# Kernel tuning notes

Hardware: AMD Instinct MI355X
Metric: run time of the kernel (lower is better)

## Reference

```python
import jax, jax.numpy as jnp
import numpy as np

L = 8      # num_hidden_layers
J = 3      # num_gnn_layers
N = 2000   # num nodes (<=2000 so prune=False)
E = 32000  # num edges
R = 64     # num relations
HID = 1024 # hidden_dim
G = 128    # gnn_dim
H = 8      # num_gnn_heads
DH = G // H          # 16 per-head dim
P = 10               # pre_seq_len
KV = 8               # plm_num_kv_heads
OUT = HID // 32 * KV # out_ft_dim = 256
B = 16               # batch (h.shape[0])


def setup_inputs() -> dict:
    key = jax.random.key(0)
    ks = jax.random.split(key, 24)
    f = lambda k, s: (jax.random.normal(k, s, dtype=jnp.float32) * 0.05)
    ri = lambda k, s, hi: jax.random.randint(k, s, 0, hi, dtype=jnp.int32)
    return {
        'nft': f(ks[0], (L, N, HID)),
        'rft': f(ks[1], (L, R, HID)),
        'importances': jax.random.normal(ks[2], (N,), dtype=jnp.float32),
        'tg_w': f(ks[3], (L, HID, G)),
        'tg_b': f(ks[4], (L, G)),
        'path_w': f(ks[5], (L, J, 3 * G, G)),
        'path_b': f(ks[6], (L, J, G)),
        'attn1_w': f(ks[7], (L, J, G, H)),
        'attn2_p': f(ks[8], (L, J, H, DH)),
        'trans_w': f(ks[9], (L, G, 2 * OUT)),
        'trans_b': f(ks[10], (L, 2 * OUT)),
        'lamda': jnp.zeros((L - 1,), dtype=jnp.float32),
        'edge_src': ri(ks[11], (E,), N),
        'edge_dst': ri(ks[12], (E,), N),
        'edge_label': ri(ks[13], (E,), R),
        'h': ri(ks[14], (B,), N),
        't': ri(ks[15], (B,), N),
    }


def _gat(x, eft, src, dst, Wp, bp, Wa1, a2p):
    # x: [N, G], eft: [E, G]
    ns = x[src]                       # [E, G] gather src node feats
    ne = x[dst]                       # [E, G] gather dst node feats
    epaths = (jnp.concatenate([ns, eft, ne], axis=-1) @ Wp + bp)
    epaths = epaths.reshape(E, H, DH)           # per-edge multi-head features
    a1 = ns @ Wa1                               # [E, H]
    a2 = jnp.einsum('ehd,hd->eh', epaths, a2p)  # [E, H]
    a = jax.nn.leaky_relu(a1 + a2)              # slope 0.01, matches torch default
    # edge softmax grouped by destination node
    amax = jax.ops.segment_max(a, dst, num_segments=N)
    ex = jnp.exp(a - amax[dst])
    ssum = jax.ops.segment_sum(ex, dst, num_segments=N)
    attn = ex / ssum[dst]                       # [E, H]
    msg = epaths * attn[..., None]              # [E, H, DH]
    agg = jax.ops.segment_sum(msg, dst, num_segments=N)  # [N, H, DH]
    return jax.nn.relu(agg.reshape(N, G) + x)


def reference(nft, rft, importances, tg_w, tg_b, path_w, path_b, attn1_w,
              attn2_p, trans_w, trans_b, lamda, edge_src, edge_dst,
              edge_label, h, t):
    bsz = h.shape[0]
    # topk indices of node importances (prune=False path)
    _, imp_idx = jax.lax.top_k(importances, P)
    pkv = []
    for i in range(L):
        x = nft[i] @ tg_w[i] + tg_b[i]                       # [N, G]
        # linear-then-gather == gather-then-linear (same math, less traffic)
        rel = rft[i] @ tg_w[i] + tg_b[i]                     # [R, G]
        gnn_eft = rel[edge_label]                            # [E, G]
        for j in range(J):
            x = _gat(x, gnn_eft, edge_src, edge_dst,
                     path_w[i, j], path_b[i, j], attn1_w[i, j], attn2_p[i, j])
        past_x = x
        if i > 0:
            s = jax.nn.sigmoid(lamda[i - 1] / 0.1)
            x = s * x + (1.0 - s) * past_x   # past_x == x (as in source)
        prefix = x[imp_idx]                                  # [P, G]
        pk = jnp.tanh(prefix) @ trans_w[i] + trans_b[i]      # [P, 2*OUT]
        pk = jnp.broadcast_to(pk[None], (bsz, P, 2 * OUT))
        pk = pk.reshape(bsz, P, 2, KV, OUT // KV).transpose(2, 0, 3, 1, 4)
        pkv.append(pk)
    return jnp.stack(pkv)   # [L, 2, B, KV, P, OUT//KV]
```

## Files before the change

### kernel.cpp

```cpp
#include <hip/hip_runtime.h>
#include <hip/hip_bf16.h>
#include <math.h>

#define L_    8
#define J_    3
#define N_    2000
#define E_    32000
#define R_    64
#define HID_  1024
#define G_    128
#define H_    8
#define DH_   16
#define P_    10
#define KV_   8
#define OUT2_ 512
#define B_    16
#define KS_   4
#define ROWS_ 2064

typedef float f32x4 __attribute__((ext_vector_type(4)));
typedef short s16x8 __attribute__((ext_vector_type(8)));

__device__ __forceinline__ void cvt_split1(float v, short& h, short& l) {
    unsigned u = __float_as_uint(v);
    h = (short)(u >> 16);
    float rem = v - __uint_as_float(u & 0xffff0000u);
    l = (short)(__float_as_uint(rem) >> 16);
}

__device__ __forceinline__ void cvt_split8(const float* v, s16x8& h, s16x8& l) {
    #pragma unroll
    for (int i = 0; i < 8; ++i) {
        unsigned u = __float_as_uint(v[i]);
        h[i] = (short)(u >> 16);
        float rem = v[i] - __uint_as_float(u & 0xffff0000u);
        l[i] = (short)(__float_as_uint(rem) >> 16);
    }
}

__global__ void k_deg(const int* __restrict__ dst, int* __restrict__ deg) {
    int e = blockIdx.x * 256 + threadIdx.x;
    if (e < E_) atomicAdd(&deg[dst[e]], 1);
}

__global__ __launch_bounds__(256) void k_scan(const int* __restrict__ deg, int* __restrict__ off) {
    __shared__ int ps[256];
    int t = threadIdx.x;
    int base = t * 8;
    int v[8];
    int sum = 0;
    #pragma unroll
    for (int j = 0; j < 8; ++j) {
        int idx = base + j;
        int d = (idx < N_) ? deg[idx] : 0;
        v[j] = sum;
        sum += d;
    }
    ps[t] = sum;
    __syncthreads();
    for (int st = 1; st < 256; st <<= 1) {
        int x = (t >= st) ? ps[t - st] : 0;
        __syncthreads();
        ps[t] += x;
        __syncthreads();
    }
    int pre = (t == 0) ? 0 : ps[t - 1];
    #pragma unroll
    for (int j = 0; j < 8; ++j) {
        int idx = base + j;
        if (idx <= N_) off[idx] = pre + v[j];
    }
}

__global__ void k_place(const int* __restrict__ dst, const int* __restrict__ src,
                        const int* __restrict__ lab, const int* __restrict__ off,
                        int* __restrict__ cur, int2* __restrict__ sl) {
    int e = blockIdx.x * 256 + threadIdx.x;
    if (e < E_) {
        int n = dst[e];
        int slot = atomicAdd(&cur[n], 1);
        sl[off[n] + slot] = make_int2(src[e], lab[e]);
    }
}

__global__ void k_topk(const float* __restrict__ imp, int* __restrict__ idx_out) {
    __shared__ float sv[N_];
    __shared__ float rv[256];
    __shared__ int   ri[256];
    int t = threadIdx.x;
    for (int i = t; i < N_; i += 256) sv[i] = imp[i];
    __syncthreads();
    for (int k = 0; k < P_; ++k) {
        float bv = -INFINITY; int bi = N_;
        for (int i = t; i < N_; i += 256) {
            float v = sv[i];
            if (v > bv || (v == bv && i < bi)) { bv = v; bi = i; }
        }
        rv[t] = bv; ri[t] = bi;
        __syncthreads();
        for (int s = 128; s > 0; s >>= 1) {
            if (t < s) {
                float v = rv[t + s]; int i2 = ri[t + s];
                if (v > rv[t] || (v == rv[t] && i2 < ri[t])) { rv[t] = v; ri[t] = i2; }
            }
            __syncthreads();
        }
        if (t == 0) { idx_out[k] = ri[0]; sv[ri[0]] = -INFINITY; }
        __syncthreads();
    }
}

__global__ __launch_bounds__(256) void k_wsplit(
    const float* __restrict__ tg_w, short* __restrict__ Wpk) {
    int layer = blockIdx.x >> 5;
    int st = blockIdx.x & 31;
    int tid = threadIdx.x;
    int col = tid & 127, khalf = tid >> 7;
    const float* src = tg_w + (size_t)layer * HID_ * G_ + (size_t)(st * 32 + khalf * 16) * G_ + col;
    short* dh = Wpk + ((size_t)(layer * 32 + st) * 2 + 0) * 4096 + tid * 16;
    short* dl = Wpk + ((size_t)(layer * 32 + st) * 2 + 1) * 4096 + tid * 16;
    #pragma unroll
    for (int kk = 0; kk < 16; ++kk) {
        short h, l;
        cvt_split1(src[(size_t)kk * G_], h, l);
        dh[kk] = h; dl[kk] = l;
    }
}

__global__ __launch_bounds__(256) void k_psplit(
    const float* __restrict__ path_w, short* __restrict__ Ppk) {
    int lj = blockIdx.x >> 3;
    int rest = blockIdx.x & 7;
    int halfc = rest >> 2;
    int st = rest & 3;
    int tid = threadIdx.x;
    int col = tid & 127, khalf = tid >> 7;
    int c0 = halfc ? 256 : 0;
    const float* src = path_w + (size_t)lj * 384 * G_ + (size_t)(c0 + st * 32 + khalf * 16) * G_ + col;
    size_t base = (((size_t)lj * 2 + halfc) * 4 + st) * 2;
    short* dh = Ppk + (base + 0) * 4096 + tid * 16;
    short* dl = Ppk + (base + 1) * 4096 + tid * 16;
    #pragma unroll
    for (int kk = 0; kk < 16; ++kk) {
        short h, l;
        cvt_split1(src[(size_t)kk * G_], h, l);
        dh[kk] = h; dl[kk] = l;
    }
}

#define TG_NS 8
__global__ __launch_bounds__(256) void k_tgA(
    const float* __restrict__ nft, const float* __restrict__ rft,
    const short* __restrict__ Wpk, float* __restrict__ part) {
    __shared__ alignas(16) short Ah[64][40];
    __shared__ alignas(16) short Al[64][40];
    __shared__ alignas(16) short Wh[128][40];
    __shared__ alignas(16) short Wl[128][40];
    const int tid = threadIdx.x;
    const int rg = blockIdx.x % 33;
    const int t2 = blockIdx.x / 33;
    const int layer = t2 % L_;
    const int ks = t2 / L_;
    const int row0 = rg * 64;
    const int k0 = ks * (HID_ / KS_);

    const int arow = tid >> 2, aq = tid & 3;
    int gra = row0 + arow; if (gra > ROWS_ - 1) gra = ROWS_ - 1;
    const float* asrc = (gra < N_)
        ? nft + ((size_t)layer * N_ + gra) * HID_ + k0
        : rft + ((size_t)layer * R_ + (gra - N_)) * HID_ + k0;
    const int wcol = tid & 127, wkh = tid >> 7;

    const int lane = tid & 63, wv = tid >> 6;
    const int lr = lane & 15, lk = (lane >> 4) * 8;

    f32x4 zero = {0.f, 0.f, 0.f, 0.f};
    f32x4 acc[4][2];
    #pragma unroll
    for (int i = 0; i < 4; ++i) { acc[i][0] = zero; acc[i][1] = zero; }

    float aa[8];
    s16x8 wh0, wh1, wl0, wl1;
    auto ldG = [&](int st) {
        int kk0 = st * 32;
        *(float4*)&aa[0] = *(const float4*)(asrc + kk0 + aq * 8);
        *(float4*)&aa[4] = *(const float4*)(asrc + kk0 + aq * 8 + 4);
        int gst = ks * TG_NS + st;
        const s16x8* ph = (const s16x8*)(Wpk + ((size_t)(layer * 32 + gst) * 2 + 0) * 4096 + tid * 16);
        const s16x8* pl = (const s16x8*)(Wpk + ((size_t)(layer * 32 + gst) * 2 + 1) * 4096 + tid * 16);
        wh0 = ph[0]; wh1 = ph[1];
        wl0 = pl[0]; wl1 = pl[1];
    };
    ldG(0);
    for (int st = 0; st < TG_NS; ++st) {
        __syncthreads();
        {
            s16x8 h, l; cvt_split8(aa, h, l);
            *(s16x8*)&Ah[arow][aq * 8] = h;
            *(s16x8*)&Al[arow][aq * 8] = l;
            *(s16x8*)&Wh[wcol][wkh * 16]     = wh0;
            *(s16x8*)&Wh[wcol][wkh * 16 + 8] = wh1;
            *(s16x8*)&Wl[wcol][wkh * 16]     = wl0;
            *(s16x8*)&Wl[wcol][wkh * 16 + 8] = wl1;
        }
        __syncthreads();
        if (st + 1 < TG_NS) ldG(st + 1);
        s16x8 bh[2], bl[2];
        #pragma unroll
        for (int c = 0; c < 2; ++c) {
            int col = wv * 32 + c * 16 + lr;
            bh[c] = *(s16x8*)&Wh[col][lk];
            bl[c] = *(s16x8*)&Wl[col][lk];
        }
        #pragma unroll
        for (int mf = 0; mf < 4; ++mf) {
            s16x8 ah = *(s16x8*)&Ah[mf * 16 + lr][lk];
            s16x8 al = *(s16x8*)&Al[mf * 16 + lr][lk];
            #pragma unroll
            for (int c = 0; c < 2; ++c) {
                acc[mf][c] = __builtin_amdgcn_mfma_f32_16x16x32_bf16(ah, bh[c], acc[mf][c], 0, 0, 0);
                acc[mf][c] = __builtin_amdgcn_mfma_f32_16x16x32_bf16(ah, bl[c], acc[mf][c], 0, 0, 0);
                acc[mf][c] = __builtin_amdgcn_mfma_f32_16x16x32_bf16(al, bh[c], acc[mf][c], 0, 0, 0);
            }
        }
    }
    float* dst = part + (size_t)(ks * L_ + layer) * ROWS_ * G_;
    const int rbase = (lane >> 4) * 4;
    #pragma unroll
    for (int mf = 0; mf < 4; ++mf) {
        #pragma unroll
        for (int c = 0; c < 2; ++c) {
            int col = wv * 32 + c * 16 + lr;
            #pragma unroll
            for (int rgi = 0; rgi < 4; ++rgi) {
                int row = row0 + mf * 16 + rbase + rgi;
                if (row < ROWS_) dst[(size_t)row * G_ + col] = acc[mf][c][rgi];
            }
        }
    }
}

__global__ __launch_bounds__(256) void k_tred(
    const float* __restrict__ part, const float* __restrict__ tg_b,
    float* __restrict__ x0, float* __restrict__ rel) {
    int f4 = blockIdx.x * 256 + threadIdx.x;
    int layer = f4 / (ROWS_ * 32);
    int rem = f4 % (ROWS_ * 32);
    int row = rem >> 5;
    int c4 = rem & 31;
    const float4* p = (const float4*)part;
    size_t stride = (size_t)L_ * ROWS_ * 32;
    size_t idx0 = ((size_t)layer * ROWS_ + row) * 32 + c4;
    float4 s0 = p[idx0];
    float4 s1 = p[idx0 + stride];
    float4 s2 = p[idx0 + 2 * stride];
    float4 s3 = p[idx0 + 3 * stride];
    float4 b = *(const float4*)(tg_b + layer * G_ + c4 * 4);
    float4 o;
    o.x = s0.x + s1.x + s2.x + s3.x + b.x;
    o.y = s0.y + s1.y + s2.y + s3.y + b.y;
    o.z = s0.z + s1.z + s2.z + s3.z + b.z;
    o.w = s0.w + s1.w + s2.w + s3.w + b.w;
    if (row < N_) ((float4*)x0)[((size_t)layer * N_ + row) * 32 + c4] = o;
    else          ((float4*)rel)[((size_t)layer * R_ + (row - N_)) * 32 + c4] = o;
}

__global__ __launch_bounds__(256) void k_prep(
    const float* __restrict__ path_w, const float* __restrict__ path_b,
    const float* __restrict__ attn1_w, const float* __restrict__ attn2_p,
    float* __restrict__ wPR, short* __restrict__ PPk, float* __restrict__ bA) {
    int j = blockIdx.x / L_;
    int l = blockIdx.x % L_;
    int t = threadIdx.x;
    size_t wb = (size_t)((l * J_ + j) * 384) * G_;
    size_t ob = (size_t)(j * L_ + l);
    const float* a2 = attn2_p + (size_t)(l * J_ + j) * G_;
    short* pph = PPk + (ob * 2 + 0) * 2048;
    short* ppl = PPk + (ob * 2 + 1) * 2048;
    for (int i = t; i < G_ * H_; i += 256) {
        int k = i >> 3, h = i & 7;
        const float* a2h = a2 + h * DH_;
        float s1 = 0.f, s2 = 0.f, s3 = 0.f;
        for (int d = 0; d < DH_; ++d) {
            float av = a2h[d];
            int c = h * DH_ + d;
            s1 += path_w[wb + (size_t)k * G_ + c] * av;
            s3 += path_w[wb + (size_t)(128 + k) * G_ + c] * av;
            s2 += path_w[wb + (size_t)(256 + k) * G_ + c] * av;
        }
        s1 += attn1_w[((size_t)(l * J_ + j) * G_ + k) * H_ + h];
        short h1, l1, h2, l2;
        cvt_split1(s1, h1, l1);
        cvt_split1(s2, h2, l2);
        pph[h * 128 + k] = h1;       ppl[h * 128 + k] = l1;
        pph[(8 + h) * 128 + k] = h2; ppl[(8 + h) * 128 + k] = l2;
        wPR[ob * H_ * G_ + h * G_ + k] = s3;
    }
    if (t < H_) {
        float s = 0.f;
        const float* a2h = a2 + t * DH_;
        const float* pb = path_b + (size_t)(l * J_ + j) * G_ + t * DH_;
        for (int d = 0; d < DH_; ++d) s += pb[d] * a2h[d];
        bA[ob * H_ + t] = s;
    }
}

__global__ __launch_bounds__(256) void k_rel(
    const float* __restrict__ rel, const float* __restrict__ path_w,
    const float* __restrict__ wPR, float* __restrict__ Rl, float* __restrict__ PR) {
    __shared__ float At[32][132];
    __shared__ float Wt[32][132];
    const int tid = threadIdx.x;
    const int halfb = blockIdx.x & 1;
    const int t2 = blockIdx.x >> 1;
    const int l = t2 % L_;
    const int j = t2 / L_;
    const int row0 = halfb * 32;
    const size_t ob = (size_t)(j * L_ + l);
    {
        int ar = tid >> 3, aq2 = tid & 7;
        const float* asrc = rel + ((size_t)l * R_ + row0 + ar) * G_ + aq2 * 16;
        float4 a0 = ((const float4*)asrc)[0], a1 = ((const float4*)asrc)[1];
        float4 a2 = ((const float4*)asrc)[2], a3 = ((const float4*)asrc)[3];
        *(float4*)&At[ar][aq2 * 16]      = a0;
        *(float4*)&At[ar][aq2 * 16 + 4]  = a1;
        *(float4*)&At[ar][aq2 * 16 + 8]  = a2;
        *(float4*)&At[ar][aq2 * 16 + 12] = a3;
    }
    const size_t wb = (size_t)((l * J_ + j) * 384) * G_;
    const int wrow = tid >> 3, wq = tid & 7;
    float4 rW0, rW1, rW2, rW3;
    auto loadW = [&](int kt) {
        const float* src = path_w + wb + (size_t)(128 + kt * 32 + wrow) * G_ + wq * 16;
        rW0 = ((const float4*)src)[0]; rW1 = ((const float4*)src)[1];
        rW2 = ((const float4*)src)[2]; rW3 = ((const float4*)src)[3];
    };
    const int tr = tid >> 4;
    const int tc = tid & 15;
    float4 acc[2][2];
    acc[0][0] = make_float4(0, 0, 0, 0); acc[0][1] = make_float4(0, 0, 0, 0);
    acc[1][0] = make_float4(0, 0, 0, 0); acc[1][1] = make_float4(0, 0, 0, 0);
    loadW(0);
    for (int wt = 0; wt < 4; ++wt) {
        __syncthreads();
        *(float4*)&Wt[wrow][wq * 16]      = rW0;
        *(float4*)&Wt[wrow][wq * 16 + 4]  = rW1;
        *(float4*)&Wt[wrow][wq * 16 + 8]  = rW2;
        *(float4*)&Wt[wrow][wq * 16 + 12] = rW3;
        __syncthreads();
        if (wt + 1 < 4) loadW(wt + 1);
        #pragma unroll
        for (int kk = 0; kk < 32; ++kk) {
            float4 w0 = *(const float4*)&Wt[kk][tc * 4];
            float4 w1 = *(const float4*)&Wt[kk][64 + tc * 4];
            float a0 = At[tr * 2][wt * 32 + kk];
            float a1 = At[tr * 2 + 1][wt * 32 + kk];
            acc[0][0].x += a0 * w0.x; acc[0][0].y += a0 * w0.y;
            acc[0][0].z += a0 * w0.z; acc[0][0].w += a0 * w0.w;
            acc[0][1].x += a0 * w1.x; acc[0][1].y += a0 * w1.y;
            acc[0][1].z += a0 * w1.z; acc[0][1].w += a0 * w1.w;
            acc[1][0].x += a1 * w0.x; acc[1][0].y += a1 * w0.y;
            acc[1][0].z += a1 * w0.z; acc[1][0].w += a1 * w0.w;
            acc[1][1].x += a1 * w1.x; acc[1][1].y += a1 * w1.y;
            acc[1][1].z += a1 * w1.z; acc[1][1].w += a1 * w1.w;
        }
    }
    #pragma unroll
    for (int r2 = 0; r2 < 2; ++r2) {
        int row = row0 + tr * 2 + r2;
        float* dst = Rl + (ob * R_ + row) * G_;
        *(float4*)(dst + tc * 4) = acc[r2][0];
        *(float4*)(dst + 64 + tc * 4) = acc[r2][1];
    }
    {
        int prow = tid >> 3, ph = tid & 7;
        const float* wp = wPR + (ob * H_ + ph) * G_;
        float s = 0.f;
        for (int k = 0; k < G_; ++k) s += At[prow][k] * wp[k];
        PR[(ob * R_ + row0 + prow) * H_ + ph] = s;
    }
}

__global__ __launch_bounds__(256) void k_proj2(
    const float* __restrict__ xcur, const short* __restrict__ Ppk,
    const short* __restrict__ PPkj, const float* __restrict__ bAj,
    const float* __restrict__ path_b, int j,
    float* __restrict__ Xs, float* __restrict__ XdB,
    float* __restrict__ PS, float* __restrict__ PDb) {
    __shared__ alignas(16) short Ah[64][40];
    __shared__ alignas(16) short Al[64][40];
    __shared__ alignas(16) short Wh[128][40];
    __shared__ alignas(16) short Wl[128][40];
    __shared__ alignas(16) short PPh[16][136];
    __shared__ alignas(16) short PPl[16][136];
    const int tid = threadIdx.x;
    const int layer = blockIdx.x & 7;
    const int rest = blockIdx.x >> 3;
    const int halfb = rest & 1;
    const int rg = rest >> 1;
    const int row0 = rg * 64;

    const int arow = tid >> 2, aq = tid & 3;
    int gra = row0 + arow; if (gra >= N_) gra = N_ - 1;
    const float* asrc = xcur + ((size_t)layer * N_ + gra) * G_;
    const int wcol = tid & 127, wkh = tid >> 7;

    const int lane = tid & 63, wv = tid >> 6;
    const int lr = lane & 15, lk = (lane >> 4) * 8;

    if (!halfb) {
        int col = tid >> 4, koff = (tid & 15) * 8;
        s16x8 vh = *(const s16x8*)(PPkj + ((size_t)layer * 2 + 0) * 2048 + tid * 8);
        s16x8 vl = *(const s16x8*)(PPkj + ((size_t)layer * 2 + 1) * 2048 + tid * 8);
        *(s16x8*)&PPh[col][koff] = vh;
        *(s16x8*)&PPl[col][koff] = vl;
    }

    f32x4 zero = {0.f, 0.f, 0.f, 0.f};
    f32x4 acc[4][2];
    f32x4 acc_pp[2];
    #pragma unroll
    for (int i = 0; i < 4; ++i) { acc[i][0] = zero; acc[i][1] = zero; }
    acc_pp[0] = zero; acc_pp[1] = zero;

    float aa[8];
    s16x8 wh0, wh1, wl0, wl1;
    const size_t pbase = (((size_t)(layer * J_ + j) * 2 + halfb) * 4) * 2;
    auto ldG = [&](int st) {
        int kk0 = st * 32;
        *(float4*)&aa[0] = *(const float4*)(asrc + kk0 + aq * 8);
        *(float4*)&aa[4] = *(const float4*)(asrc + kk0 + aq * 8 + 4);
        const s16x8* ph = (const s16x8*)(Ppk + (pbase + (size_t)st * 2 + 0) * 4096 + tid * 16);
        const s16x8* pl = (const s16x8*)(Ppk + (pbase + (size_t)st * 2 + 1) * 4096 + tid * 16);
        wh0 = ph[0]; wh1 = ph[1];
        wl0 = pl[0]; wl1 = pl[1];
    };
    ldG(0);
    for (int st = 0; st < 4; ++st) {
        __syncthreads();
        {
            s16x8 h, l; cvt_split8(aa, h, l);
            *(s16x8*)&Ah[arow][aq * 8] = h;
            *(s16x8*)&Al[arow][aq * 8] = l;
            *(s16x8*)&Wh[wcol][wkh * 16]     = wh0;
            *(s16x8*)&Wh[wcol][wkh * 16 + 8] = wh1;
            *(s16x8*)&Wl[wcol][wkh * 16]     = wl0;
            *(s16x8*)&Wl[wcol][wkh * 16 + 8] = wl1;
        }
        __syncthreads();
        if (st + 1 < 4) ldG(st + 1);
        s16x8 bh[2], bl[2];
        #pragma unroll
        for (int c = 0; c < 2; ++c) {
            int col = wv * 32 + c * 16 + lr;
            bh[c] = *(s16x8*)&Wh[col][lk];
            bl[c] = *(s16x8*)&Wl[col][lk];
        }
        s16x8 ppb_h, ppb_l;
        if (!halfb) {
            ppb_h = *(s16x8*)&PPh[lr][st * 32 + lk];
            ppb_l = *(s16x8*)&PPl[lr][st * 32 + lk];
        }
        #pragma unroll
        for (int mf = 0; mf < 4; ++mf) {
            s16x8 ah = *(s16x8*)&Ah[mf * 16 + lr][lk];
            s16x8 al = *(s16x8*)&Al[mf * 16 + lr][lk];
            #pragma unroll
            for (int c = 0; c < 2; ++c) {
                acc[mf][c] = __builtin_amdgcn_mfma_f32_16x16x32_bf16(ah, bh[c], acc[mf][c], 0, 0, 0);
                acc[mf][c] = __builtin_amdgcn_mfma_f32_16x16x32_bf16(ah, bl[c], acc[mf][c], 0, 0, 0);
                acc[mf][c] = __builtin_amdgcn_mfma_f32_16x16x32_bf16(al, bh[c], acc[mf][c], 0, 0, 0);
            }
            if (!halfb && (mf >> 1) == wv) {
                int i = mf & 1;
                acc_pp[i] = __builtin_amdgcn_mfma_f32_16x16x32_bf16(ah, ppb_h, acc_pp[i], 0, 0, 0);
                acc_pp[i] = __builtin_amdgcn_mfma_f32_16x16x32_bf16(ah, ppb_l, acc_pp[i], 0, 0, 0);
                acc_pp[i] = __builtin_amdgcn_mfma_f32_16x16x32_bf16(al, ppb_h, acc_pp[i], 0, 0, 0);
            }
        }
    }
    const float* pb = path_b + (size_t)(layer * J_ + j) * G_;
    float* outp = halfb ? XdB : Xs;
    const int rbase = (lane >> 4) * 4;
    #pragma unroll
    for (int mf = 0; mf < 4; ++mf) {
        #pragma unroll
        for (int c = 0; c < 2; ++c) {
            int col = wv * 32 + c * 16 + lr;
            float bias = halfb ? pb[col] : 0.f;
            #pragma unroll
            for (int rgi = 0; rgi < 4; ++rgi) {
                int row = row0 + mf * 16 + rbase + rgi;
                if (row < N_) outp[((size_t)layer * N_ + row) * G_ + col] = acc[mf][c][rgi] + bias;
            }
        }
    }
    if (!halfb) {
        #pragma unroll
        for (int i = 0; i < 2; ++i) {
            int mf = wv * 2 + i;
            #pragma unroll
            for (int rgi = 0; rgi < 4; ++rgi) {
                int row = row0 + mf * 16 + rbase + rgi;
                if (row >= N_) continue;
                float val = acc_pp[i][rgi];
                if (lr < 8) PS[((size_t)layer * N_ + row) * H_ + lr] = val;
                else        PDb[((size_t)layer * N_ + row) * H_ + (lr - 8)] = val + bAj[layer * H_ + (lr - 8)];
            }
        }
    }
}

__global__ __launch_bounds__(256) void k_node(
    const float* __restrict__ xcur, const float* __restrict__ Xs,
    const float* __restrict__ XdB, const float* __restrict__ Rlj,
    const float* __restrict__ PS, const float* __restrict__ PDb,
    const float* __restrict__ PRj,
    const int* __restrict__ off, const int2* __restrict__ csr_sl,
    float* __restrict__ xnext) {
    int l = blockIdx.x & 7;
    int n = (blockIdx.x >> 3) * 4 + (threadIdx.x >> 6);
    int lane = threadIdx.x & 63;
    int o0 = off[n], o1 = off[n + 1];
    const float* xr = xcur + ((size_t)l * N_ + n) * G_;
    float xv0 = xr[lane], xv1 = xr[lane + 64];
    float xd0 = XdB[((size_t)l * N_ + n) * G_ + lane];
    float xd1 = XdB[((size_t)l * N_ + n) * G_ + lane + 64];
    float out0, out1;
    if (o1 == o0) {
        out0 = fmaxf(xv0, 0.f);
        out1 = fmaxf(xv1, 0.f);
    } else {
        const int h0 = lane >> 4, h1 = h0 + 4;
        const float pd0 = PDb[((size_t)l * N_ + n) * H_ + h0];
        const float pd1 = PDb[((size_t)l * N_ + n) * H_ + h1];
        const float* PSl = PS + (size_t)l * N_ * H_;
        const float* PRl = PRj + (size_t)l * R_ * H_;
        const float* Xsl = Xs + (size_t)l * N_ * G_;
        const float* Rll = Rlj + (size_t)l * R_ * G_;
        float acc0 = 0.f, acc1 = 0.f, sum0 = 0.f, sum1 = 0.f;
        #pragma unroll 2
        for (int k = o0; k < o1; ++k) {
            int2 sl = csr_sl[k];
            float lg0 = PSl[sl.x * H_ + h0] + PRl[sl.y * H_ + h0] + pd0;
            float lg1 = PSl[sl.x * H_ + h1] + PRl[sl.y * H_ + h1] + pd1;
            lg0 = (lg0 >= 0.f) ? lg0 : 0.01f * lg0;
            lg1 = (lg1 >= 0.f) ? lg1 : 0.01f * lg1;
            float e0 = __expf(lg0), e1 = __expf(lg1);
            float v0 = Xsl[(size_t)sl.x * G_ + lane]      + Rll[(size_t)sl.y * G_ + lane];
            float v1 = Xsl[(size_t)sl.x * G_ + lane + 64] + Rll[(size_t)sl.y * G_ + lane + 64];
            acc0 += e0 * v0; sum0 += e0;
            acc1 += e1 * v1; sum1 += e1;
        }
        out0 = fmaxf(acc0 / sum0 + xd0 + xv0, 0.f);
        out1 = fmaxf(acc1 / sum1 + xd1 + xv1, 0.f);
    }
    float* dst = xnext + ((size_t)l * N_ + n) * G_;
    dst[lane] = out0;
    dst[lane + 64] = out1;
}

__global__ __launch_bounds__(256) void k_out(
    const float* __restrict__ xfin, const int* __restrict__ imp_idx,
    const float* __restrict__ trans_w, const float* __restrict__ trans_b,
    float* __restrict__ out) {
    int blk = blockIdx.x;
    int layer = blk / P_, p = blk % P_;
    __shared__ float th[G_];
    int t = threadIdx.x;
    int row = imp_idx[p];
    if (t < G_) th[t] = tanhf(xfin[((size_t)layer * N_ + row) * G_ + t]);
    __syncthreads();
    for (int c = t; c < OUT2_; c += 256) {
        float s = trans_b[layer * OUT2_ + c];
        const float* W = trans_w + (size_t)layer * G_ * OUT2_ + c;
        for (int k = 0; k < G_; ++k) s += th[k] * W[(size_t)k * OUT2_];
        int c2 = c >> 8, kv = (c >> 5) & 7, oo = c & 31;
        for (int b = 0; b < B_; ++b) {
            out[(((((size_t)layer * 2 + c2) * B_ + b) * KV_ + kv) * P_ + p) * 32 + oo] = s;
        }
    }
}

extern "C" void kernel_launch(void* const* d_in, const int* in_sizes, int n_in,
                              void* d_out, int out_size, void* d_ws, size_t ws_size,
                              hipStream_t stream) {
    const float* nft     = (const float*)d_in[0];
    const float* rft     = (const float*)d_in[1];
    const float* imp     = (const float*)d_in[2];
    const float* tg_w    = (const float*)d_in[3];
    const float* tg_b    = (const float*)d_in[4];
    const float* path_w  = (const float*)d_in[5];
    const float* path_b  = (const float*)d_in[6];
    const float* attn1_w = (const float*)d_in[7];
    const float* attn2_p = (const float*)d_in[8];
    const float* trans_w = (const float*)d_in[9];
    const float* trans_b = (const float*)d_in[10];
    const int* esrc = (const int*)d_in[12];
    const int* edst = (const int*)d_in[13];
    const int* elab = (const int*)d_in[14];
    float* out = (float*)d_out;

    char* w = (char*)d_ws;
    size_t off = 0;
    auto alloc = [&](size_t bytes) {
        void* p = w + off;
        off += (bytes + 255) & ~(size_t)255;
        return p;
    };
    float* part    = (float*)alloc((size_t)KS_ * L_ * ROWS_ * G_ * 4);
    float* x0      = (float*)alloc((size_t)L_ * N_ * G_ * 4);
    float* x1      = (float*)alloc((size_t)L_ * N_ * G_ * 4);
    float* rel     = (float*)alloc((size_t)L_ * R_ * G_ * 4);
    float* Xs      = (float*)alloc((size_t)L_ * N_ * G_ * 4);
    float* XdB     = (float*)alloc((size_t)L_ * N_ * G_ * 4);
    float* Rl      = (float*)alloc((size_t)J_ * L_ * R_ * G_ * 4);
    float* PS      = (float*)alloc((size_t)L_ * N_ * H_ * 4);
    float* PDb     = (float*)alloc((size_t)L_ * N_ * H_ * 4);
    float* PR      = (float*)alloc((size_t)J_ * L_ * R_ * H_ * 4);
    float* wPR     = (float*)alloc((size_t)J_ * L_ * H_ * G_ * 4);
    float* bA      = (float*)alloc((size_t)J_ * L_ * H_ * 4);
    short* Wpk     = (short*)alloc((size_t)L_ * 32 * 2 * 4096 * 2);
    short* Ppk     = (short*)alloc((size_t)L_ * J_ * 2 * 4 * 2 * 4096 * 2);
    short* PPk     = (short*)alloc((size_t)J_ * L_ * 2 * 2048 * 2);
    int*   deg     = (int*)alloc(N_ * 4);
    int*   cur     = (int*)alloc(N_ * 4);
    int*   csr_off = (int*)alloc((N_ + 1) * 4);
    int2*  csr_sl  = (int2*)alloc((size_t)E_ * 8);
    int*   imp_idx = (int*)alloc(P_ * 4);

    hipMemsetAsync(deg, 0, N_ * 4, stream);
    hipMemsetAsync(cur, 0, N_ * 4, stream);

    k_deg<<<E_ / 256, 256, 0, stream>>>(edst, deg);
    k_scan<<<1, 256, 0, stream>>>(deg, csr_off);
    k_place<<<E_ / 256, 256, 0, stream>>>(edst, esrc, elab, csr_off, cur, csr_sl);
    k_topk<<<1, 256, 0, stream>>>(imp, imp_idx);

    k_wsplit<<<L_ * 32, 256, 0, stream>>>(tg_w, Wpk);
    k_psplit<<<L_ * J_ * 2 * 4, 256, 0, stream>>>(path_w, Ppk);

    k_tgA<<<KS_ * L_ * 33, 256, 0, stream>>>(nft, rft, Wpk, part);
    k_tred<<<2064, 256, 0, stream>>>(part, tg_b, x0, rel);

    k_prep<<<J_ * L_, 256, 0, stream>>>(path_w, path_b, attn1_w, attn2_p,
                                        wPR, PPk, bA);
    k_rel<<<J_ * L_ * 2, 256, 0, stream>>>(rel, path_w, wPR, Rl, PR);

    float* xc = x0;
    float* xn = x1;
    for (int j = 0; j < J_; ++j) {
        k_proj2<<<L_ * 32 * 2, 256, 0, stream>>>(
            xc, Ppk, PPk + (size_t)j * L_ * 2 * 2048, bA + (size_t)j * L_ * H_,
            path_b, j, Xs, XdB, PS, PDb);
        k_node<<<L_ * 500, 256, 0, stream>>>(
            xc, Xs, XdB, Rl + (size_t)j * L_ * R_ * G_, PS, PDb,
            PR + (size_t)j * L_ * R_ * H_,
            csr_off, csr_sl, xn);
        float* tmp = xc; xc = xn; xn = tmp;
    }
    k_out<<<L_ * P_, 256, 0, stream>>>(xc, imp_idx, trans_w, trans_b, out);
}
```

Baseline: 227.6 us.

## Merge preprocessing kernels and replace split-K tg GEMM with direct-register full-K MFMA

```diff
diff --git a/kernel.cpp b/kernel.cpp
--- a/kernel.cpp
+++ b/kernel.cpp
@@ -15,7 +15,6 @@
 #define KV_   8
 #define OUT2_ 512
 #define B_    16
-#define KS_   4
 #define ROWS_ 2064
 
 typedef float f32x4 __attribute__((ext_vector_type(4)));
@@ -38,12 +37,27 @@
     }
 }
 
-__global__ void k_deg(const int* __restrict__ dst, int* __restrict__ deg) {
-    int e = blockIdx.x * 256 + threadIdx.x;
+__device__ __forceinline__ void cvt_split8v(float4 a, float4 b, s16x8& h, s16x8& l) {
+    short hh, ll;
+    cvt_split1(a.x, hh, ll); h[0] = hh; l[0] = ll;
+    cvt_split1(a.y, hh, ll); h[1] = hh; l[1] = ll;
+    cvt_split1(a.z, hh, ll); h[2] = hh; l[2] = ll;
+    cvt_split1(a.w, hh, ll); h[3] = hh; l[3] = ll;
+    cvt_split1(b.x, hh, ll); h[4] = hh; l[4] = ll;
+    cvt_split1(b.y, hh, ll); h[5] = hh; l[5] = ll;
+    cvt_split1(b.z, hh, ll); h[6] = hh; l[6] = ll;
+    cvt_split1(b.w, hh, ll); h[7] = hh; l[7] = ll;
+}
+
+
+__device__ __forceinline__ void deg_body(int b, const int* __restrict__ dst,
+                                         int* __restrict__ deg) {
+    int e = b * 256 + threadIdx.x;
     if (e < E_) atomicAdd(&deg[dst[e]], 1);
 }
 
-__global__ __launch_bounds__(256) void k_scan(const int* __restrict__ deg, int* __restrict__ off) {
+__device__ __forceinline__ void scan_body(const int* __restrict__ deg,
+                                          int* __restrict__ off) {
     __shared__ int ps[256];
     int t = threadIdx.x;
     int base = t * 8;
@@ -72,10 +86,13 @@
     }
 }
 
-__global__ void k_place(const int* __restrict__ dst, const int* __restrict__ src,
-                        const int* __restrict__ lab, const int* __restrict__ off,
-                        int* __restrict__ cur, int2* __restrict__ sl) {
-    int e = blockIdx.x * 256 + threadIdx.x;
+__device__ __forceinline__ void place_body(int b, const int* __restrict__ dst,
+                                           const int* __restrict__ src,
+                                           const int* __restrict__ lab,
+                                           const int* __restrict__ off,
+                                           int* __restrict__ cur,
+                                           int2* __restrict__ sl) {
+    int e = b * 256 + threadIdx.x;
     if (e < E_) {
         int n = dst[e];
         int slot = atomicAdd(&cur[n], 1);
@@ -83,7 +100,8 @@
     }
 }
 
-__global__ void k_topk(const float* __restrict__ imp, int* __restrict__ idx_out) {
+__device__ __forceinline__ void topk_body(const float* __restrict__ imp,
+                                          int* __restrict__ idx_out) {
     __shared__ float sv[N_];
     __shared__ float rv[256];
     __shared__ int   ri[256];
@@ -110,15 +128,15 @@
     }
 }
 
-__global__ __launch_bounds__(256) void k_wsplit(
-    const float* __restrict__ tg_w, short* __restrict__ Wpk) {
-    int layer = blockIdx.x >> 5;
-    int st = blockIdx.x & 31;
+__device__ __forceinline__ void wsplitB_body(int b, const float* __restrict__ tg_w,
+                                             short* __restrict__ WpkB) {
+    int layer = b >> 5;
+    int gst = b & 31;
     int tid = threadIdx.x;
     int col = tid & 127, khalf = tid >> 7;
-    const float* src = tg_w + (size_t)layer * HID_ * G_ + (size_t)(st * 32 + khalf * 16) * G_ + col;
-    short* dh = Wpk + ((size_t)(layer * 32 + st) * 2 + 0) * 4096 + tid * 16;
-    short* dl = Wpk + ((size_t)(layer * 32 + st) * 2 + 1) * 4096 + tid * 16;
+    const float* src = tg_w + ((size_t)layer * HID_ + gst * 32 + khalf * 16) * G_ + col;
+    short* dh = WpkB + ((size_t)(layer * 32 + gst) * 2 + 0) * 4096 + col * 32 + khalf * 16;
+    short* dl = WpkB + ((size_t)(layer * 32 + gst) * 2 + 1) * 4096 + col * 32 + khalf * 16;
     #pragma unroll
     for (int kk = 0; kk < 16; ++kk) {
         short h, l;
@@ -127,10 +145,10 @@
     }
 }
 
-__global__ __launch_bounds__(256) void k_psplit(
-    const float* __restrict__ path_w, short* __restrict__ Ppk) {
-    int lj = blockIdx.x >> 3;
-    int rest = blockIdx.x & 7;
+__device__ __forceinline__ void psplit_body(int b, const float* __restrict__ path_w,
+                                            short* __restrict__ Ppk) {
+    int lj = b >> 3;
+    int rest = b & 7;
     int halfc = rest >> 2;
     int st = rest & 3;
     int tid = threadIdx.x;
@@ -148,129 +166,15 @@
     }
 }
 
-#define TG_NS 8
-__global__ __launch_bounds__(256) void k_tgA(
-    const float* __restrict__ nft, const float* __restrict__ rft,
-    const short* __restrict__ Wpk, float* __restrict__ part) {
-    __shared__ alignas(16) short Ah[64][40];
-    __shared__ alignas(16) short Al[64][40];
-    __shared__ alignas(16) short Wh[128][40];
-    __shared__ alignas(16) short Wl[128][40];
-    const int tid = threadIdx.x;
-    const int rg = blockIdx.x % 33;
-    const int t2 = blockIdx.x / 33;
-    const int layer = t2 % L_;
-    const int ks = t2 / L_;
-    const int row0 = rg * 64;
-    const int k0 = ks * (HID_ / KS_);
-
-    const int arow = tid >> 2, aq = tid & 3;
-    int gra = row0 + arow; if (gra > ROWS_ - 1) gra = ROWS_ - 1;
-    const float* asrc = (gra < N_)
-        ? nft + ((size_t)layer * N_ + gra) * HID_ + k0
-        : rft + ((size_t)layer * R_ + (gra - N_)) * HID_ + k0;
-    const int wcol = tid & 127, wkh = tid >> 7;
-
-    const int lane = tid & 63, wv = tid >> 6;
-    const int lr = lane & 15, lk = (lane >> 4) * 8;
-
-    f32x4 zero = {0.f, 0.f, 0.f, 0.f};
-    f32x4 acc[4][2];
-    #pragma unroll
-    for (int i = 0; i < 4; ++i) { acc[i][0] = zero; acc[i][1] = zero; }
-
-    float aa[8];
-    s16x8 wh0, wh1, wl0, wl1;
-    auto ldG = [&](int st) {
-        int kk0 = st * 32;
-        *(float4*)&aa[0] = *(const float4*)(asrc + kk0 + aq * 8);
-        *(float4*)&aa[4] = *(const float4*)(asrc + kk0 + aq * 8 + 4);
-        int gst = ks * TG_NS + st;
-        const s16x8* ph = (const s16x8*)(Wpk + ((size_t)(layer * 32 + gst) * 2 + 0) * 4096 + tid * 16);
-        const s16x8* pl = (const s16x8*)(Wpk + ((size_t)(layer * 32 + gst) * 2 + 1) * 4096 + tid * 16);
-        wh0 = ph[0]; wh1 = ph[1];
-        wl0 = pl[0]; wl1 = pl[1];
-    };
-    ldG(0);
-    for (int st = 0; st < TG_NS; ++st) {
-        __syncthreads();
-        {
-            s16x8 h, l; cvt_split8(aa, h, l);
-            *(s16x8*)&Ah[arow][aq * 8] = h;
-            *(s16x8*)&Al[arow][aq * 8] = l;
-            *(s16x8*)&Wh[wcol][wkh * 16]     = wh0;
-            *(s16x8*)&Wh[wcol][wkh * 16 + 8] = wh1;
-            *(s16x8*)&Wl[wcol][wkh * 16]     = wl0;
-            *(s16x8*)&Wl[wcol][wkh * 16 + 8] = wl1;
-        }
-        __syncthreads();
-        if (st + 1 < TG_NS) ldG(st + 1);
-        s16x8 bh[2], bl[2];
-        #pragma unroll
-        for (int c = 0; c < 2; ++c) {
-            int col = wv * 32 + c * 16 + lr;
-            bh[c] = *(s16x8*)&Wh[col][lk];
-            bl[c] = *(s16x8*)&Wl[col][lk];
-        }
-        #pragma unroll
-        for (int mf = 0; mf < 4; ++mf) {
-            s16x8 ah = *(s16x8*)&Ah[mf * 16 + lr][lk];
-            s16x8 al = *(s16x8*)&Al[mf * 16 + lr][lk];
-            #pragma unroll
-            for (int c = 0; c < 2; ++c) {
-                acc[mf][c] = __builtin_amdgcn_mfma_f32_16x16x32_bf16(ah, bh[c], acc[mf][c], 0, 0, 0);
-                acc[mf][c] = __builtin_amdgcn_mfma_f32_16x16x32_bf16(ah, bl[c], acc[mf][c], 0, 0, 0);
-                acc[mf][c] = __builtin_amdgcn_mfma_f32_16x16x32_bf16(al, bh[c], acc[mf][c], 0, 0, 0);
-            }
-        }
-    }
-    float* dst = part + (size_t)(ks * L_ + layer) * ROWS_ * G_;
-    const int rbase = (lane >> 4) * 4;
-    #pragma unroll
-    for (int mf = 0; mf < 4; ++mf) {
-        #pragma unroll
-        for (int c = 0; c < 2; ++c) {
-            int col = wv * 32 + c * 16 + lr;
-            #pragma unroll
-            for (int rgi = 0; rgi < 4; ++rgi) {
-                int row = row0 + mf * 16 + rbase + rgi;
-                if (row < ROWS_) dst[(size_t)row * G_ + col] = acc[mf][c][rgi];
-            }
-        }
-    }
-}
-
-__global__ __launch_bounds__(256) void k_tred(
-    const float* __restrict__ part, const float* __restrict__ tg_b,
-    float* __restrict__ x0, float* __restrict__ rel) {
-    int f4 = blockIdx.x * 256 + threadIdx.x;
-    int layer = f4 / (ROWS_ * 32);
-    int rem = f4 % (ROWS_ * 32);
-    int row = rem >> 5;
-    int c4 = rem & 31;
-    const float4* p = (const float4*)part;
-    size_t stride = (size_t)L_ * ROWS_ * 32;
-    size_t idx0 = ((size_t)layer * ROWS_ + row) * 32 + c4;
-    float4 s0 = p[idx0];
-    float4 s1 = p[idx0 + stride];
-    float4 s2 = p[idx0 + 2 * stride];
-    float4 s3 = p[idx0 + 3 * stride];
-    float4 b = *(const float4*)(tg_b + layer * G_ + c4 * 4);
-    float4 o;
-    o.x = s0.x + s1.x + s2.x + s3.x + b.x;
-    o.y = s0.y + s1.y + s2.y + s3.y + b.y;
-    o.z = s0.z + s1.z + s2.z + s3.z + b.z;
-    o.w = s0.w + s1.w + s2.w + s3.w + b.w;
-    if (row < N_) ((float4*)x0)[((size_t)layer * N_ + row) * 32 + c4] = o;
-    else          ((float4*)rel)[((size_t)layer * R_ + (row - N_)) * 32 + c4] = o;
-}
-
-__global__ __launch_bounds__(256) void k_prep(
-    const float* __restrict__ path_w, const float* __restrict__ path_b,
-    const float* __restrict__ attn1_w, const float* __restrict__ attn2_p,
-    float* __restrict__ wPR, short* __restrict__ PPk, float* __restrict__ bA) {
-    int j = blockIdx.x / L_;
-    int l = blockIdx.x % L_;
+__device__ __forceinline__ void prep_body(int b, const float* __restrict__ path_w,
+                                          const float* __restrict__ path_b,
+                                          const float* __restrict__ attn1_w,
+                                          const float* __restrict__ attn2_p,
+                                          float* __restrict__ wPR,
+                                          short* __restrict__ PPk,
+                                          float* __restrict__ bA) {
+    int j = b / L_;
+    int l = b % L_;
     int t = threadIdx.x;
     size_t wb = (size_t)((l * J_ + j) * 384) * G_;
     size_t ob = (size_t)(j * L_ + l);
@@ -303,6 +207,132 @@
         for (int d = 0; d < DH_; ++d) s += pb[d] * a2h[d];
         bA[ob * H_ + t] = s;
     }
+}
+
+__device__ __forceinline__ void tg_body(
+    int b, const float* __restrict__ nft, const float* __restrict__ rft,
+    const short* __restrict__ WpkB, const float* __restrict__ tg_b,
+    float* __restrict__ x0, float* __restrict__ rel) {
+    const int layer = b & 7;
+    const int rg = b >> 3;
+    const int row0 = rg * 32;
+    const int tid = threadIdx.x;
+    const int lane = tid & 63, wv = tid >> 6;
+    const int lr = lane & 15, kg = lane >> 4;
+
+    const float* aptr[2];
+    #pragma unroll
+    for (int mf = 0; mf < 2; ++mf) {
+        int r = row0 + mf * 16 + lr;
+        if (r > ROWS_ - 1) r = ROWS_ - 1;
+        aptr[mf] = (r < N_)
+            ? nft + ((size_t)layer * N_ + r) * HID_ + kg * 8
+            : rft + ((size_t)layer * R_ + (r - N_)) * HID_ + kg * 8;
+    }
+    const short* bptr = WpkB + (size_t)layer * 32 * 8192 + (wv * 32 + lr) * 32 + kg * 8;
+
+    f32x4 zero = {0.f, 0.f, 0.f, 0.f};
+    f32x4 acc[2][2];
+    acc[0][0] = zero; acc[0][1] = zero; acc[1][0] = zero; acc[1][1] = zero;
+
+    float4 a4[2][2][2];
+    s16x8  bb[2][2][2];
+
+#define TG_LOAD(S, GST) do { \
+    _Pragma("unroll") \
+    for (int mf_ = 0; mf_ < 2; ++mf_) { \
+        const float4* p4_ = (const float4*)(aptr[mf_] + (size_t)(GST) * 32); \
+        a4[S][mf_][0] = p4_[0]; \
+        a4[S][mf_][1] = p4_[1]; \
+    } \
+    const short* bp_ = bptr + (size_t)(GST) * 8192; \
+    _Pragma("unroll") \
+    for (int n_ = 0; n_ < 2; ++n_) { \
+        _Pragma("unroll") \
+        for (int p_ = 0; p_ < 2; ++p_) \
+            bb[S][n_][p_] = *(const s16x8*)(bp_ + p_ * 4096 + n_ * 512); \
+    } \
+} while (0)
+
+#define TG_COMP(S) do { \
+    _Pragma("unroll") \
+    for (int mf_ = 0; mf_ < 2; ++mf_) { \
+        s16x8 ah_, al_; \
+        cvt_split8v(a4[S][mf_][0], a4[S][mf_][1], ah_, al_); \
+        _Pragma("unroll") \
+        for (int n_ = 0; n_ < 2; ++n_) { \
+            acc[mf_][n_] = __builtin_amdgcn_mfma_f32_16x16x32_bf16(ah_, bb[S][n_][0], acc[mf_][n_], 0, 0, 0); \
+            acc[mf_][n_] = __builtin_amdgcn_mfma_f32_16x16x32_bf16(ah_, bb[S][n_][1], acc[mf_][n_], 0, 0, 0); \
+            acc[mf_][n_] = __builtin_amdgcn_mfma_f32_16x16x32_bf16(al_, bb[S][n_][0], acc[mf_][n_], 0, 0, 0); \
+        } \
+    } \
+} while (0)
+
+    TG_LOAD(0, 0);
+    for (int t = 0; t < 30; t += 2) {
+        TG_LOAD(1, t + 1);
+        TG_COMP(0);
+        TG_LOAD(0, t + 2);
+        TG_COMP(1);
+    }
+    TG_LOAD(1, 31);
+    TG_COMP(0);
+    TG_COMP(1);
+#undef TG_LOAD
+#undef TG_COMP
+
+    const int rb = kg * 4;
+    #pragma unroll
+    for (int n = 0; n < 2; ++n) {
+        int col = wv * 32 + n * 16 + lr;
+        float bias = tg_b[layer * G_ + col];
+        #pragma unroll
+        for (int mf = 0; mf < 2; ++mf) {
+            #pragma unroll
+            for (int rgi = 0; rgi < 4; ++rgi) {
+                int row = row0 + mf * 16 + rb + rgi;
+                if (row >= ROWS_) continue;
+                float v = acc[mf][n][rgi] + bias;
+                if (row < N_) x0[((size_t)layer * N_ + row) * G_ + col] = v;
+                else          rel[((size_t)layer * R_ + (row - N_)) * G_ + col] = v;
+            }
+        }
+    }
+}
+
+
+__global__ __launch_bounds__(256) void k_pre1(
+    const int* __restrict__ edst, const float* __restrict__ imp,
+    const float* __restrict__ tg_w, const float* __restrict__ path_w,
+    int* __restrict__ deg, int* __restrict__ imp_idx,
+    short* __restrict__ WpkB, short* __restrict__ Ppk) {
+    int b = blockIdx.x;
+    if (b < 125) { deg_body(b, edst, deg); return; }
+    if (b == 125) { topk_body(imp, imp_idx); return; }
+    if (b < 382) { wsplitB_body(b - 126, tg_w, WpkB); return; }
+    psplit_body(b - 382, path_w, Ppk);
+}
+
+__global__ __launch_bounds__(256) void k_pre2(
+    const int* __restrict__ deg, const float* __restrict__ path_w,
+    const float* __restrict__ path_b, const float* __restrict__ attn1_w,
+    const float* __restrict__ attn2_p, int* __restrict__ csr_off,
+    float* __restrict__ wPR, short* __restrict__ PPk, float* __restrict__ bA) {
+    int b = blockIdx.x;
+    if (b == 0) { scan_body(deg, csr_off); return; }
+    prep_body(b - 1, path_w, path_b, attn1_w, attn2_p, wPR, PPk, bA);
+}
+
+__global__ __launch_bounds__(256) void k_pre3(
+    const int* __restrict__ edst, const int* __restrict__ esrc,
+    const int* __restrict__ elab, const int* __restrict__ off,
+    int* __restrict__ cur, int2* __restrict__ csr_sl,
+    const float* __restrict__ nft, const float* __restrict__ rft,
+    const short* __restrict__ WpkB, const float* __restrict__ tg_b,
+    float* __restrict__ x0, float* __restrict__ rel) {
+    int b = blockIdx.x;
+    if (b < 125) { place_body(b, edst, esrc, elab, off, cur, csr_sl); return; }
+    tg_body(b - 125, nft, rft, WpkB, tg_b, x0, rel);
 }
 
 __global__ __launch_bounds__(256) void k_rel(
@@ -608,7 +638,6 @@
         off += (bytes + 255) & ~(size_t)255;
         return p;
     };
-    float* part    = (float*)alloc((size_t)KS_ * L_ * ROWS_ * G_ * 4);
     float* x0      = (float*)alloc((size_t)L_ * N_ * G_ * 4);
     float* x1      = (float*)alloc((size_t)L_ * N_ * G_ * 4);
     float* rel     = (float*)alloc((size_t)L_ * R_ * G_ * 4);
@@ -632,19 +661,13 @@
     hipMemsetAsync(deg, 0, N_ * 4, stream);
     hipMemsetAsync(cur, 0, N_ * 4, stream);
 
-    k_deg<<<E_ / 256, 256, 0, stream>>>(edst, deg);
-    k_scan<<<1, 256, 0, stream>>>(deg, csr_off);
-    k_place<<<E_ / 256, 256, 0, stream>>>(edst, esrc, elab, csr_off, cur, csr_sl);
-    k_topk<<<1, 256, 0, stream>>>(imp, imp_idx);
-
-    k_wsplit<<<L_ * 32, 256, 0, stream>>>(tg_w, Wpk);
-    k_psplit<<<L_ * J_ * 2 * 4, 256, 0, stream>>>(path_w, Ppk);
-
-    k_tgA<<<KS_ * L_ * 33, 256, 0, stream>>>(nft, rft, Wpk, part);
-    k_tred<<<2064, 256, 0, stream>>>(part, tg_b, x0, rel);
-
-    k_prep<<<J_ * L_, 256, 0, stream>>>(path_w, path_b, attn1_w, attn2_p,
-                                        wPR, PPk, bA);
+    k_pre1<<<125 + 1 + 256 + 192, 256, 0, stream>>>(
+        edst, imp, tg_w, path_w, deg, imp_idx, Wpk, Ppk);
+    k_pre2<<<1 + 24, 256, 0, stream>>>(
+        deg, path_w, path_b, attn1_w, attn2_p, csr_off, wPR, PPk, bA);
+    k_pre3<<<125 + 520, 256, 0, stream>>>(
+        edst, esrc, elab, csr_off, cur, csr_sl, nft, rft, Wpk, tg_b, x0, rel);
+
     k_rel<<<J_ * L_ * 2, 256, 0, stream>>>(rel, path_w, wPR, Rl, PR);
 
     float* xc = x0;
```

New measurement: 245.9 us. +8.0%, slower.
